# Performance work log

Hardware: AMD Instinct MI355X
Metric: run time of the kernel (lower is better)

The kernel has to match this reference:

```python
import jax, jax.numpy as jnp
import numpy as np

H, W = 5, 11          # fixed spatial map from ConvLSTM2D((5,11), ...)
P = H * W             # 55 pixels; 1x1 convs are per-pixel linear layers
HC = 64               # hidden channels
IC = 2                # input channels
FC_DIMS = [2 * HC * P, 3400, 1000, 500, 50]  # 7040 -> 3400 -> 1000 -> 500 -> 50


def setup_inputs() -> dict:
    key = jax.random.key(0)
    ks = jax.random.split(key, 24)
    B, T = 32, 256
    s = 0.05
    d = {}
    d["x1"] = jax.random.normal(ks[0], (B, T, IC, H, W), jnp.float32)
    d["x2"] = jax.random.normal(ks[1], (B, T, IC, H, W), jnp.float32)
    # ConvLSTM cell params: 1x1 convs fused into (in, 4*HC) matrices, gate order i,f,o,g
    d["wx1"] = jax.random.normal(ks[2], (IC, 4 * HC), jnp.float32) * s
    d["wh1"] = jax.random.normal(ks[3], (HC, 4 * HC), jnp.float32) * s
    d["bx1"] = jax.random.normal(ks[4], (4 * HC,), jnp.float32) * s
    d["bh1"] = jax.random.normal(ks[5], (4 * HC,), jnp.float32) * s
    d["wx2"] = jax.random.normal(ks[6], (IC, 4 * HC), jnp.float32) * s
    d["wh2"] = jax.random.normal(ks[7], (HC, 4 * HC), jnp.float32) * s
    d["bx2"] = jax.random.normal(ks[8], (4 * HC,), jnp.float32) * s
    d["bh2"] = jax.random.normal(ks[9], (4 * HC,), jnp.float32) * s
    # FC stack (stored as (in,out) so y = x @ W + b, equivalent to torch Linear)
    for i in range(4):
        fan_in, fan_out = FC_DIMS[i], FC_DIMS[i + 1]
        lim = 1.0 / np.sqrt(fan_in)
        d[f"fw{i+2}"] = jax.random.uniform(ks[10 + 2 * i], (fan_in, fan_out), jnp.float32, -lim, lim)
        d[f"fb{i+2}"] = jax.random.uniform(ks[11 + 2 * i], (fan_out,), jnp.float32, -lim, lim)
    return d


def _cell_step(h, c, gx, wh, bh):
    # gx: (B,P,4*HC) precomputed x contribution; h,c: (B,P,HC)
    g = gx + h @ wh + bh
    i, f, o, gg = jnp.split(g, 4, axis=-1)
    c = jax.nn.sigmoid(f) * c + jax.nn.sigmoid(i) * jnp.tanh(gg)
    h = jax.nn.sigmoid(o) * jnp.tanh(c)
    return h, c


def _sub_forward(x, wx1, wh1, bx1, bh1, wx2, wh2, bx2, bh2,
                 fw2, fb2, fw3, fb3, fw4, fb4, fw5, fb5):
    B, T = x.shape[0], x.shape[1]
    # (B,T,C,H,W) -> (B,T,P,C): pixels become a batch dim for the 1x1 convs
    xs = x.transpose(0, 1, 3, 4, 2).reshape(B, T, P, IC)
    # Precompute all input-to-gate projections once (big batched GEMM)
    gx1 = jnp.einsum('btpc,cd->btpd', xs, wx1) + bx1            # cell1: forward in time
    gx2 = jnp.einsum('btpc,cd->btpd', xs[:, ::-1], wx2) + bx2   # cell2: reversed in time
    h0 = jnp.zeros((B, P, HC), x.dtype)

    def step(carry, g):
        h1, c1, h2, c2 = carry
        g1, g2 = g
        h1, c1 = _cell_step(h1, c1, g1, wh1, bh1)
        h2, c2 = _cell_step(h2, c2, g2, wh2, bh2)
        return (h1, c1, h2, c2), None

    (h1, _, h2, _), _ = jax.lax.scan(
        step, (h0, h0, h0, h0),
        (gx1.transpose(1, 0, 2, 3), gx2.transpose(1, 0, 2, 3)))

    # torch.cat((h1,h2),1) on (B,HC,H,W) then flatten -> channel-major layout
    out = jnp.concatenate([h1.transpose(0, 2, 1), h2.transpose(0, 2, 1)], axis=1).reshape(B, -1)
    out = out @ fw2 + fb2
    out = out @ fw3 + fb3
    out = out @ fw4 + fb4
    out = out @ fw5 + fb5
    return out


def reference(x1, x2, wx1, wh1, bx1, bh1, wx2, wh2, bx2, bh2,
              fw2, fb2, fw3, fb3, fw4, fb4, fw5, fb5):
    args = (wx1, wh1, bx1, bh1, wx2, wh2, bx2, bh2,
            fw2, fb2, fw3, fb3, fw4, fb4, fw5, fb5)
    out1 = _sub_forward(x1, *args)
    out2 = _sub_forward(x2, *args)
    return (out1, out2)
```

## Files before the change

kernel.cpp:

```cpp
#include <hip/hip_runtime.h>


#define T_STEPS 256
#define PIX 55
#define MT 16
#define TILES 110
#define LOG2E 1.4426950408889634f
#define FC_SUB 128
#define FC_GRP 16

typedef float f32x4 __attribute__((ext_vector_type(4)));
typedef __bf16 bf16x8 __attribute__((ext_vector_type(8)));
typedef __bf16 bf16x4 __attribute__((ext_vector_type(4)));

__global__ __launch_bounds__(256) void lstm_kernel(
    const float* __restrict__ x1, const float* __restrict__ x2,
    const float* __restrict__ wx1, const float* __restrict__ wh1,
    const float* __restrict__ bx1, const float* __restrict__ bh1,
    const float* __restrict__ wx2, const float* __restrict__ wh2,
    const float* __restrict__ bx2, const float* __restrict__ bh2,
    float* __restrict__ feat)
{
    int bid  = blockIdx.x;
    int tile = bid % TILES;
    int cc   = bid / TILES;
    int sub  = cc >> 1, cell = cc & 1;
    const float* x  = sub  ? x2  : x1;
    const float* wx = cell ? wx2 : wx1;
    const float* wh = cell ? wh2 : wh1;
    const float* bx = cell ? bx2 : bx1;
    const float* bh = cell ? bh2 : bh1;

    int tid  = threadIdx.x;
    int w    = tid >> 6;
    int l    = tid & 63;
    int quad = l >> 4;
    int c16  = l & 15;

    __shared__ float xl[MT * 514];
    __shared__ __align__(16) __bf16 hb[2][2][MT][72];

    {
        int seq0 = tile * MT;
        for (int i = 0; i < 32; ++i) {
            int idx = tid + 256 * i;
            int m = idx >> 9;
            int tc = idx & 511;
            int t = tc >> 1, c = tc & 1;
            int seq = seq0 + m;
            int b = seq / PIX, p = seq % PIX;
            xl[m * 514 + tc] = x[((b * T_STEPS + t) * 2 + c) * PIX + p];
        }
    }
    {
        __bf16* hz = &hb[0][0][0][0];
        for (int i = tid; i < 2 * 2 * MT * 72; i += 256) hz[i] = (__bf16)0.0f;
    }

    bf16x8 Whi[4][2], Wlo[4][2];
    float btot[4][4], wxa[4][4], wxb[4][4];
#pragma unroll
    for (int g = 0; g < 4; ++g) {
        int col = 64 * g + 16 * w + c16;
#pragma unroll
        for (int r = 0; r < 4; ++r) {
            int u = 64 * g + 16 * w + 4 * quad + r;
            btot[g][r] = bx[u] + bh[u];
            wxa[g][r]  = wx[u];
            wxb[g][r]  = wx[256 + u];
        }
#pragma unroll
        for (int q = 0; q < 2; ++q) {
#pragma unroll
            for (int j = 0; j < 8; ++j) {
                int k = 32 * q + 8 * quad + j;
                float wv = wh[k * 256 + col];
                __bf16 hi = (__bf16)wv;
                Whi[g][q][j] = hi;
                Wlo[g][q][j] = (__bf16)(wv - (float)hi);
            }
        }
    }

    float cst[4]  = {0.f, 0.f, 0.f, 0.f};
    float hfin[4] = {0.f, 0.f, 0.f, 0.f};

    __syncthreads();
    float2 xv = *(const float2*)&xl[c16 * 514 + (cell ? (T_STEPS - 1) : 0) * 2];

#pragma unroll 2
    for (int t = 0; t < T_STEPS; ++t) {
        int rb = t & 1, wb = rb ^ 1;

        bf16x8 Bh[2], Bl[2];
#pragma unroll
        for (int q = 0; q < 2; ++q) {
            Bh[q] = *(const bf16x8*)&hb[rb][0][c16][32 * q + 8 * quad];
            Bl[q] = *(const bf16x8*)&hb[rb][1][c16][32 * q + 8 * quad];
        }

        f32x4 acc[4];
#pragma unroll
        for (int g = 0; g < 4; ++g) {
#pragma unroll
            for (int r = 0; r < 4; ++r)
                acc[g][r] = fmaf(xv.y, wxb[g][r], fmaf(xv.x, wxa[g][r], btot[g][r]));
        }
#pragma unroll
        for (int g = 0; g < 4; ++g)
            acc[g] = __builtin_amdgcn_mfma_f32_16x16x32_bf16(Whi[g][0], Bh[0], acc[g], 0, 0, 0);
#pragma unroll
        for (int g = 0; g < 4; ++g)
            acc[g] = __builtin_amdgcn_mfma_f32_16x16x32_bf16(Whi[g][1], Bh[1], acc[g], 0, 0, 0);
#pragma unroll
        for (int g = 0; g < 4; ++g)
            acc[g] = __builtin_amdgcn_mfma_f32_16x16x32_bf16(Wlo[g][0], Bh[0], acc[g], 0, 0, 0);
#pragma unroll
        for (int g = 0; g < 4; ++g)
            acc[g] = __builtin_amdgcn_mfma_f32_16x16x32_bf16(Wlo[g][1], Bh[1], acc[g], 0, 0, 0);
#pragma unroll
        for (int g = 0; g < 4; ++g)
            acc[g] = __builtin_amdgcn_mfma_f32_16x16x32_bf16(Whi[g][0], Bl[0], acc[g], 0, 0, 0);
#pragma unroll
        for (int g = 0; g < 4; ++g)
            acc[g] = __builtin_amdgcn_mfma_f32_16x16x32_bf16(Whi[g][1], Bl[1], acc[g], 0, 0, 0);

        float ei[4], ef[4], eo[4], eg[4];
#pragma unroll
        for (int r = 0; r < 4; ++r) {
            ei[r] = __builtin_amdgcn_exp2f(-LOG2E * acc[0][r]);
            ef[r] = __builtin_amdgcn_exp2f(-LOG2E * acc[1][r]);
            eo[r] = __builtin_amdgcn_exp2f(-LOG2E * acc[2][r]);
            eg[r] = __builtin_amdgcn_exp2f(-2.0f * LOG2E * acc[3][r]);
        }

        bf16x4 ph, pl;
#pragma unroll
        for (int r = 0; r < 4; ++r) {
            float sf  = __builtin_amdgcn_rcpf(1.0f + ef[r]);
            float itg = (1.0f - eg[r]) * __builtin_amdgcn_rcpf((1.0f + ei[r]) * (1.0f + eg[r]));
            float c   = fmaf(sf, cst[r], itg);
            cst[r] = c;
            float ec = __builtin_amdgcn_exp2f(-2.0f * LOG2E * c);
            float h  = (1.0f - ec) * __builtin_amdgcn_rcpf((1.0f + eo[r]) * (1.0f + ec));
            hfin[r] = h;
            __bf16 hi = (__bf16)h;
            ph[r] = hi;
            pl[r] = (__bf16)(h - (float)hi);
        }
        *(bf16x4*)&hb[wb][0][c16][16 * w + 4 * quad] = ph;
        *(bf16x4*)&hb[wb][1][c16][16 * w + 4 * quad] = pl;

        {
            int txn = (cell ? (T_STEPS - 2 - t) : (t + 1)) & 255;
            xv = *(const float2*)&xl[c16 * 514 + txn * 2];
        }
        __syncthreads();
    }

    {
        int seq = tile * MT + c16;
        int b = seq / PIX, p = seq % PIX;
#pragma unroll
        for (int r = 0; r < 4; ++r) {
            int u = 16 * w + 4 * quad + r;
            feat[(size_t)(sub * 32 + b) * 7040 + (cell * 64 + u) * PIX + p] = hfin[r];
        }
    }
}

__global__ __launch_bounds__(256) void fc_init(
    const float* __restrict__ b2, const float* __restrict__ b3,
    const float* __restrict__ b4, const float* __restrict__ b5,
    float* __restrict__ t1, float* __restrict__ t2,
    float* __restrict__ t3, float* __restrict__ o)
{
    int i = blockIdx.x * 256 + threadIdx.x;
    const int n1 = 64 * 3400, n2 = 64 * 1000, n3 = 64 * 500, n4 = 64 * 50;
    if (i < n1) { t1[i] = b2[i % 3400]; return; }
    i -= n1;
    if (i < n2) { t2[i] = b3[i % 1000]; return; }
    i -= n2;
    if (i < n3) { t3[i] = b4[i % 500]; return; }
    i -= n3;
    if (i < n4) { o[i] = b5[i % 50]; }
}

__global__ __launch_bounds__(256) void fc_gemm(const float* __restrict__ A,
                                               const float* __restrict__ W,
                                               float* __restrict__ out,
                                               int K, int N, int kchunk) {
    __shared__ __align__(16) float al[FC_SUB * 68];
    int tid = threadIdx.x;
    int l   = tid & 63;
    int wv  = tid >> 6;
    int k0   = blockIdx.y * kchunk;
    int kend = min(K, k0 + kchunk);

    int n  = blockIdx.x * 64 + l;
    int ne = min(n, N - 1);

    float acc[16];
#pragma unroll
    for (int i = 0; i < 16; ++i) acc[i] = 0.0f;

    for (int ks = k0; ks < kend; ks += FC_SUB) {
        int kcur = min(FC_SUB, kend - ks);
        __syncthreads();
        if (kcur == FC_SUB) {
#pragma unroll
            for (int i = 0; i < 32; ++i) {
                int idx = tid + 256 * i;
                int m = idx >> 7, kc = idx & 127;
                al[kc * 68 + m] = A[(size_t)m * K + ks + kc];
            }
        } else {
#pragma unroll
            for (int i = 0; i < 32; ++i) {
                int idx = tid + 256 * i;
                int m = idx >> 7, kc = idx & 127;
                if (kc < kcur) al[kc * 68 + m] = A[(size_t)m * K + ks + kc];
            }
        }
        __syncthreads();

        const float* wr = W + (size_t)ks * N + ne;
        if (kcur == FC_SUB) {
#pragma unroll
            for (int g8 = 0; g8 < FC_SUB / FC_GRP; ++g8) {
                float wbuf[FC_GRP];
#pragma unroll
                for (int j = 0; j < FC_GRP; ++j)
                    wbuf[j] = wr[(size_t)(g8 * FC_GRP + j) * N];
#pragma unroll
                for (int j = 0; j < FC_GRP; ++j) {
                    const float4* ap = (const float4*)&al[(g8 * FC_GRP + j) * 68 + 16 * wv];
#pragma unroll
                    for (int i = 0; i < 4; ++i) {
                        float4 a = ap[i];
                        acc[4 * i + 0] = fmaf(a.x, wbuf[j], acc[4 * i + 0]);
                        acc[4 * i + 1] = fmaf(a.y, wbuf[j], acc[4 * i + 1]);
                        acc[4 * i + 2] = fmaf(a.z, wbuf[j], acc[4 * i + 2]);
                        acc[4 * i + 3] = fmaf(a.w, wbuf[j], acc[4 * i + 3]);
                    }
                }
            }
        } else {
            int kc0 = 0;
            for (; kc0 + FC_GRP <= kcur; kc0 += FC_GRP) {
                float wbuf[FC_GRP];
#pragma unroll
                for (int j = 0; j < FC_GRP; ++j)
                    wbuf[j] = wr[(size_t)(kc0 + j) * N];
#pragma unroll
                for (int j = 0; j < FC_GRP; ++j) {
                    const float4* ap = (const float4*)&al[(kc0 + j) * 68 + 16 * wv];
#pragma unroll
                    for (int i = 0; i < 4; ++i) {
                        float4 a = ap[i];
                        acc[4 * i + 0] = fmaf(a.x, wbuf[j], acc[4 * i + 0]);
                        acc[4 * i + 1] = fmaf(a.y, wbuf[j], acc[4 * i + 1]);
                        acc[4 * i + 2] = fmaf(a.z, wbuf[j], acc[4 * i + 2]);
                        acc[4 * i + 3] = fmaf(a.w, wbuf[j], acc[4 * i + 3]);
                    }
                }
            }
            for (; kc0 < kcur; ++kc0) {
                float wvv = wr[(size_t)kc0 * N];
                const float4* ap = (const float4*)&al[kc0 * 68 + 16 * wv];
#pragma unroll
                for (int i = 0; i < 4; ++i) {
                    float4 a = ap[i];
                    acc[4 * i + 0] = fmaf(a.x, wvv, acc[4 * i + 0]);
                    acc[4 * i + 1] = fmaf(a.y, wvv, acc[4 * i + 1]);
                    acc[4 * i + 2] = fmaf(a.z, wvv, acc[4 * i + 2]);
                    acc[4 * i + 3] = fmaf(a.w, wvv, acc[4 * i + 3]);
                }
            }
        }
    }

    if (n < N) {
        float* pr = out + n;
#pragma unroll
        for (int i = 0; i < 16; ++i)
            unsafeAtomicAdd(&pr[(size_t)(16 * wv + i) * N], acc[i]);
    }
}

extern "C" void kernel_launch(void* const* d_in, const int* in_sizes, int n_in,
                              void* d_out, int out_size, void* d_ws, size_t ws_size,
                              hipStream_t stream) {
    const float* x1  = (const float*)d_in[0];
    const float* x2  = (const float*)d_in[1];
    const float* wx1 = (const float*)d_in[2];
    const float* wh1 = (const float*)d_in[3];
    const float* bx1 = (const float*)d_in[4];
    const float* bh1 = (const float*)d_in[5];
    const float* wx2 = (const float*)d_in[6];
    const float* wh2 = (const float*)d_in[7];
    const float* bx2 = (const float*)d_in[8];
    const float* bh2 = (const float*)d_in[9];
    const float* fw2 = (const float*)d_in[10];
    const float* fb2 = (const float*)d_in[11];
    const float* fw3 = (const float*)d_in[12];
    const float* fb3 = (const float*)d_in[13];
    const float* fw4 = (const float*)d_in[14];
    const float* fb4 = (const float*)d_in[15];
    const float* fw5 = (const float*)d_in[16];
    const float* fb5 = (const float*)d_in[17];

    char* ws = (char*)d_ws;
    float* feat = (float*)ws;
    float* t1   = feat + (size_t)64 * 7040;
    float* t2   = t1   + (size_t)64 * 3400;
    float* t3   = t2   + (size_t)64 * 1000;
    float* o    = (float*)d_out;

    fc_init<<<dim3(1238), dim3(256), 0, stream>>>(fb2, fb3, fb4, fb5, t1, t2, t3, o);

    lstm_kernel<<<dim3(440), dim3(256), 0, stream>>>(
        x1, x2, wx1, wh1, bx1, bh1, wx2, wh2, bx2, bh2, feat);

    fc_gemm<<<dim3(54, 28), dim3(256), 0, stream>>>(feat, fw2, t1, 7040, 3400, 256);
    fc_gemm<<<dim3(16, 54), dim3(256), 0, stream>>>(t1, fw3, t2, 3400, 1000, 64);
    fc_gemm<<<dim3(8, 16), dim3(256), 0, stream>>>(t2, fw4, t3, 1000, 500, 64);
    fc_gemm<<<dim3(1, 16), dim3(256), 0, stream>>>(t3, fw5, o, 500, 50, 32);
}
```

Baseline: 550.8 us.

## Halve LSTM block to two waves, each computing two 16-unit subtiles per gate

The recurrent LSTM kernel now runs with 128 threads (2 wavefronts) instead of 256. Each wave owns 32 hidden units per gate as two 16-column subtiles, which doubles the per-wave MFMA and activation work and the register-resident weights. The aim is to cut block-wide barrier cost per timestep and let the scheduler interleave independent MFMA chains. In exchange, register pressure doubles and per-step latency per wave grows, with fewer waves available to hide latency.

```diff
diff --git a/kernel.cpp b/kernel.cpp
--- a/kernel.cpp
+++ b/kernel.cpp
@@ -13,7 +13,7 @@
 typedef __bf16 bf16x8 __attribute__((ext_vector_type(8)));
 typedef __bf16 bf16x4 __attribute__((ext_vector_type(4)));
 
-__global__ __launch_bounds__(256) void lstm_kernel(
+__global__ __launch_bounds__(128, 1) void lstm_kernel(
     const float* __restrict__ x1, const float* __restrict__ x2,
     const float* __restrict__ wx1, const float* __restrict__ wh1,
     const float* __restrict__ bx1, const float* __restrict__ bh1,
@@ -32,7 +32,7 @@
     const float* bh = cell ? bh2 : bh1;
 
     int tid  = threadIdx.x;
-    int w    = tid >> 6;
+    int wv   = tid >> 6;
     int l    = tid & 63;
     int quad = l >> 4;
     int c16  = l & 15;
@@ -42,8 +42,8 @@
 
     {
         int seq0 = tile * MT;
-        for (int i = 0; i < 32; ++i) {
-            int idx = tid + 256 * i;
+        for (int i = 0; i < 64; ++i) {
+            int idx = tid + 128 * i;
             int m = idx >> 9;
             int tc = idx & 511;
             int t = tc >> 1, c = tc & 1;
@@ -54,36 +54,39 @@
     }
     {
         __bf16* hz = &hb[0][0][0][0];
-        for (int i = tid; i < 2 * 2 * MT * 72; i += 256) hz[i] = (__bf16)0.0f;
-    }
-
-    bf16x8 Whi[4][2], Wlo[4][2];
-    float btot[4][4], wxa[4][4], wxb[4][4];
+        for (int i = tid; i < 2 * 2 * MT * 72; i += 128) hz[i] = (__bf16)0.0f;
+    }
+
+    bf16x8 Whi[4][2][2], Wlo[4][2][2];
+    float btot[4][2][4], wxa[4][2][4], wxb[4][2][4];
 #pragma unroll
     for (int g = 0; g < 4; ++g) {
-        int col = 64 * g + 16 * w + c16;
-#pragma unroll
-        for (int r = 0; r < 4; ++r) {
-            int u = 64 * g + 16 * w + 4 * quad + r;
-            btot[g][r] = bx[u] + bh[u];
-            wxa[g][r]  = wx[u];
-            wxb[g][r]  = wx[256 + u];
-        }
-#pragma unroll
-        for (int q = 0; q < 2; ++q) {
-#pragma unroll
-            for (int j = 0; j < 8; ++j) {
-                int k = 32 * q + 8 * quad + j;
-                float wv = wh[k * 256 + col];
-                __bf16 hi = (__bf16)wv;
-                Whi[g][q][j] = hi;
-                Wlo[g][q][j] = (__bf16)(wv - (float)hi);
-            }
-        }
-    }
-
-    float cst[4]  = {0.f, 0.f, 0.f, 0.f};
-    float hfin[4] = {0.f, 0.f, 0.f, 0.f};
+#pragma unroll
+        for (int s = 0; s < 2; ++s) {
+            int col = 64 * g + 32 * wv + 16 * s + c16;
+#pragma unroll
+            for (int r = 0; r < 4; ++r) {
+                int u = 64 * g + 32 * wv + 16 * s + 4 * quad + r;
+                btot[g][s][r] = bx[u] + bh[u];
+                wxa[g][s][r]  = wx[u];
+                wxb[g][s][r]  = wx[256 + u];
+            }
+#pragma unroll
+            for (int q = 0; q < 2; ++q) {
+#pragma unroll
+                for (int j = 0; j < 8; ++j) {
+                    int k = 32 * q + 8 * quad + j;
+                    float wvv = wh[k * 256 + col];
+                    __bf16 hi = (__bf16)wvv;
+                    Whi[g][s][q][j] = hi;
+                    Wlo[g][s][q][j] = (__bf16)(wvv - (float)hi);
+                }
+            }
+        }
+    }
+
+    float cst[2][4]  = {{0.f, 0.f, 0.f, 0.f}, {0.f, 0.f, 0.f, 0.f}};
+    float hfin[2][4] = {{0.f, 0.f, 0.f, 0.f}, {0.f, 0.f, 0.f, 0.f}};
 
     __syncthreads();
     float2 xv = *(const float2*)&xl[c16 * 514 + (cell ? (T_STEPS - 1) : 0) * 2];
@@ -99,57 +102,80 @@
             Bl[q] = *(const bf16x8*)&hb[rb][1][c16][32 * q + 8 * quad];
         }
 
-        f32x4 acc[4];
-#pragma unroll
-        for (int g = 0; g < 4; ++g) {
-#pragma unroll
-            for (int r = 0; r < 4; ++r)
-                acc[g][r] = fmaf(xv.y, wxb[g][r], fmaf(xv.x, wxa[g][r], btot[g][r]));
-        }
-#pragma unroll
-        for (int g = 0; g < 4; ++g)
-            acc[g] = __builtin_amdgcn_mfma_f32_16x16x32_bf16(Whi[g][0], Bh[0], acc[g], 0, 0, 0);
-#pragma unroll
-        for (int g = 0; g < 4; ++g)
-            acc[g] = __builtin_amdgcn_mfma_f32_16x16x32_bf16(Whi[g][1], Bh[1], acc[g], 0, 0, 0);
-#pragma unroll
-        for (int g = 0; g < 4; ++g)
-            acc[g] = __builtin_amdgcn_mfma_f32_16x16x32_bf16(Wlo[g][0], Bh[0], acc[g], 0, 0, 0);
-#pragma unroll
-        for (int g = 0; g < 4; ++g)
-            acc[g] = __builtin_amdgcn_mfma_f32_16x16x32_bf16(Wlo[g][1], Bh[1], acc[g], 0, 0, 0);
-#pragma unroll
-        for (int g = 0; g < 4; ++g)
-            acc[g] = __builtin_amdgcn_mfma_f32_16x16x32_bf16(Whi[g][0], Bl[0], acc[g], 0, 0, 0);
-#pragma unroll
-        for (int g = 0; g < 4; ++g)
-            acc[g] = __builtin_amdgcn_mfma_f32_16x16x32_bf16(Whi[g][1], Bl[1], acc[g], 0, 0, 0);
-
-        float ei[4], ef[4], eo[4], eg[4];
-#pragma unroll
-        for (int r = 0; r < 4; ++r) {
-            ei[r] = __builtin_amdgcn_exp2f(-LOG2E * acc[0][r]);
-            ef[r] = __builtin_amdgcn_exp2f(-LOG2E * acc[1][r]);
-            eo[r] = __builtin_amdgcn_exp2f(-LOG2E * acc[2][r]);
-            eg[r] = __builtin_amdgcn_exp2f(-2.0f * LOG2E * acc[3][r]);
-        }
-
-        bf16x4 ph, pl;
-#pragma unroll
-        for (int r = 0; r < 4; ++r) {
-            float sf  = __builtin_amdgcn_rcpf(1.0f + ef[r]);
-            float itg = (1.0f - eg[r]) * __builtin_amdgcn_rcpf((1.0f + ei[r]) * (1.0f + eg[r]));
-            float c   = fmaf(sf, cst[r], itg);
-            cst[r] = c;
-            float ec = __builtin_amdgcn_exp2f(-2.0f * LOG2E * c);
-            float h  = (1.0f - ec) * __builtin_amdgcn_rcpf((1.0f + eo[r]) * (1.0f + ec));
-            hfin[r] = h;
-            __bf16 hi = (__bf16)h;
-            ph[r] = hi;
-            pl[r] = (__bf16)(h - (float)hi);
-        }
-        *(bf16x4*)&hb[wb][0][c16][16 * w + 4 * quad] = ph;
-        *(bf16x4*)&hb[wb][1][c16][16 * w + 4 * quad] = pl;
+        f32x4 acc[4][2];
+#pragma unroll
+        for (int g = 0; g < 4; ++g)
+#pragma unroll
+            for (int s = 0; s < 2; ++s)
+#pragma unroll
+                for (int r = 0; r < 4; ++r)
+                    acc[g][s][r] = fmaf(xv.y, wxb[g][s][r],
+                                        fmaf(xv.x, wxa[g][s][r], btot[g][s][r]));
+
+#pragma unroll
+        for (int g = 0; g < 4; ++g)
+#pragma unroll
+            for (int s = 0; s < 2; ++s)
+                acc[g][s] = __builtin_amdgcn_mfma_f32_16x16x32_bf16(Whi[g][s][0], Bh[0], acc[g][s], 0, 0, 0);
+#pragma unroll
+        for (int g = 0; g < 4; ++g)
+#pragma unroll
+            for (int s = 0; s < 2; ++s)
+                acc[g][s] = __builtin_amdgcn_mfma_f32_16x16x32_bf16(Whi[g][s][1], Bh[1], acc[g][s], 0, 0, 0);
+#pragma unroll
+        for (int g = 0; g < 4; ++g)
+#pragma unroll
+            for (int s = 0; s < 2; ++s)
+                acc[g][s] = __builtin_amdgcn_mfma_f32_16x16x32_bf16(Wlo[g][s][0], Bh[0], acc[g][s], 0, 0, 0);
+#pragma unroll
+        for (int g = 0; g < 4; ++g)
+#pragma unroll
+            for (int s = 0; s < 2; ++s)
+                acc[g][s] = __builtin_amdgcn_mfma_f32_16x16x32_bf16(Wlo[g][s][1], Bh[1], acc[g][s], 0, 0, 0);
+#pragma unroll
+        for (int g = 0; g < 4; ++g)
+#pragma unroll
+            for (int s = 0; s < 2; ++s)
+                acc[g][s] = __builtin_amdgcn_mfma_f32_16x16x32_bf16(Whi[g][s][0], Bl[0], acc[g][s], 0, 0, 0);
+#pragma unroll
+        for (int g = 0; g < 4; ++g)
+#pragma unroll
+            for (int s = 0; s < 2; ++s)
+                acc[g][s] = __builtin_amdgcn_mfma_f32_16x16x32_bf16(Whi[g][s][1], Bl[1], acc[g][s], 0, 0, 0);
+
+        float ei[2][4], ef[2][4], eo[2][4], eg[2][4];
+#pragma unroll
+        for (int s = 0; s < 2; ++s)
+#pragma unroll
+            for (int r = 0; r < 4; ++r) {
+                ei[s][r] = __builtin_amdgcn_exp2f(-LOG2E * acc[0][s][r]);
+                ef[s][r] = __builtin_amdgcn_exp2f(-LOG2E * acc[1][s][r]);
+                eo[s][r] = __builtin_amdgcn_exp2f(-LOG2E * acc[2][s][r]);
+                eg[s][r] = __builtin_amdgcn_exp2f(-2.0f * LOG2E * acc[3][s][r]);
+            }
+
+        bf16x4 ph[2], pl[2];
+#pragma unroll
+        for (int s = 0; s < 2; ++s)
+#pragma unroll
+            for (int r = 0; r < 4; ++r) {
+                float sf  = __builtin_amdgcn_rcpf(1.0f + ef[s][r]);
+                float itg = (1.0f - eg[s][r]) *
+                            __builtin_amdgcn_rcpf((1.0f + ei[s][r]) * (1.0f + eg[s][r]));
+                float c   = fmaf(sf, cst[s][r], itg);
+                cst[s][r] = c;
+                float ec = __builtin_amdgcn_exp2f(-2.0f * LOG2E * c);
+                float h  = (1.0f - ec) * __builtin_amdgcn_rcpf((1.0f + eo[s][r]) * (1.0f + ec));
+                hfin[s][r] = h;
+                __bf16 hi = (__bf16)h;
+                ph[s][r] = hi;
+                pl[s][r] = (__bf16)(h - (float)hi);
+            }
+#pragma unroll
+        for (int s = 0; s < 2; ++s) {
+            *(bf16x4*)&hb[wb][0][c16][32 * wv + 16 * s + 4 * quad] = ph[s];
+            *(bf16x4*)&hb[wb][1][c16][32 * wv + 16 * s + 4 * quad] = pl[s];
+        }
 
         {
             int txn = (cell ? (T_STEPS - 2 - t) : (t + 1)) & 255;
@@ -162,10 +188,12 @@
         int seq = tile * MT + c16;
         int b = seq / PIX, p = seq % PIX;
 #pragma unroll
-        for (int r = 0; r < 4; ++r) {
-            int u = 16 * w + 4 * quad + r;
-            feat[(size_t)(sub * 32 + b) * 7040 + (cell * 64 + u) * PIX + p] = hfin[r];
-        }
+        for (int s = 0; s < 2; ++s)
+#pragma unroll
+            for (int r = 0; r < 4; ++r) {
+                int u = 32 * wv + 16 * s + 4 * quad + r;
+                feat[(size_t)(sub * 32 + b) * 7040 + (cell * 64 + u) * PIX + p] = hfin[s][r];
+            }
     }
 }
 
@@ -319,7 +347,7 @@
 
     fc_init<<<dim3(1238), dim3(256), 0, stream>>>(fb2, fb3, fb4, fb5, t1, t2, t3, o);
 
-    lstm_kernel<<<dim3(440), dim3(256), 0, stream>>>(
+    lstm_kernel<<<dim3(440), dim3(128), 0, stream>>>(
         x1, x2, wx1, wh1, bx1, bh1, wx2, wh2, bx2, bh2, feat);
 
     fc_gemm<<<dim3(54, 28), dim3(256), 0, stream>>>(feat, fw2, t1, 7040, 3400, 256);
```

Measured after the change: 585.0 us. 6.2% more time.

## Fold bias-init into LSTM launch and prescale gate weights by exp constants

Applied to the files above, without the earlier changes.

Drops the separate fc_init kernel by adding 10 extra blocks to the LSTM launch that write the FC bias broadcasts with a grid-stride loop, saving one launch. Also folds the -log2e and -2*log2e sigmoid/tanh scaling into the recurrent weights, input weights and biases at load time, which removes four multiplies per gate element from the serial recurrence. Prescaling changes how the split bf16 hi/lo weights round, with a small numerical difference. The init blocks take CU slots alongside the 440 LSTM blocks.

```diff
diff --git a/kernel.cpp b/kernel.cpp
--- a/kernel.cpp
+++ b/kernel.cpp
@@ -5,6 +5,8 @@
 #define PIX 55
 #define MT 16
 #define TILES 110
+#define LSTM_BLOCKS 440
+#define INIT_BLOCKS 10
 #define LOG2E 1.4426950408889634f
 #define FC_SUB 128
 #define FC_GRP 16
@@ -19,9 +21,31 @@
     const float* __restrict__ bx1, const float* __restrict__ bh1,
     const float* __restrict__ wx2, const float* __restrict__ wh2,
     const float* __restrict__ bx2, const float* __restrict__ bh2,
-    float* __restrict__ feat)
+    float* __restrict__ feat,
+    const float* __restrict__ fb2, const float* __restrict__ fb3,
+    const float* __restrict__ fb4, const float* __restrict__ fb5,
+    float* __restrict__ t1, float* __restrict__ t2,
+    float* __restrict__ t3, float* __restrict__ o)
 {
     int bid  = blockIdx.x;
+    int tid  = threadIdx.x;
+
+    if (bid >= LSTM_BLOCKS) {
+        int base = (bid - LSTM_BLOCKS) * 256 + tid;
+        const int n1 = 64 * 3400, n2 = 64 * 1000, n3 = 64 * 500, n4 = 64 * 50;
+        const int tot = n1 + n2 + n3 + n4;
+        for (int i = base; i < tot; i += 256 * INIT_BLOCKS) {
+            int j = i;
+            if (j < n1) { t1[j] = fb2[j % 3400]; continue; }
+            j -= n1;
+            if (j < n2) { t2[j] = fb3[j % 1000]; continue; }
+            j -= n2;
+            if (j < n3) { t3[j] = fb4[j % 500]; continue; }
+            o[j - n3] = fb5[(j - n3) % 50];
+        }
+        return;
+    }
+
     int tile = bid % TILES;
     int cc   = bid / TILES;
     int sub  = cc >> 1, cell = cc & 1;
@@ -31,7 +55,6 @@
     const float* bx = cell ? bx2 : bx1;
     const float* bh = cell ? bh2 : bh1;
 
-    int tid  = threadIdx.x;
     int w    = tid >> 6;
     int l    = tid & 63;
     int quad = l >> 4;
@@ -61,20 +84,21 @@
     float btot[4][4], wxa[4][4], wxb[4][4];
 #pragma unroll
     for (int g = 0; g < 4; ++g) {
+        float sg = (g == 3) ? (-2.0f * LOG2E) : (-LOG2E);
         int col = 64 * g + 16 * w + c16;
 #pragma unroll
         for (int r = 0; r < 4; ++r) {
             int u = 64 * g + 16 * w + 4 * quad + r;
-            btot[g][r] = bx[u] + bh[u];
-            wxa[g][r]  = wx[u];
-            wxb[g][r]  = wx[256 + u];
+            btot[g][r] = sg * (bx[u] + bh[u]);
+            wxa[g][r]  = sg * wx[u];
+            wxb[g][r]  = sg * wx[256 + u];
         }
 #pragma unroll
         for (int q = 0; q < 2; ++q) {
 #pragma unroll
             for (int j = 0; j < 8; ++j) {
                 int k = 32 * q + 8 * quad + j;
-                float wv = wh[k * 256 + col];
+                float wv = sg * wh[k * 256 + col];
                 __bf16 hi = (__bf16)wv;
                 Whi[g][q][j] = hi;
                 Wlo[g][q][j] = (__bf16)(wv - (float)hi);
@@ -128,10 +152,10 @@
         float ei[4], ef[4], eo[4], eg[4];
 #pragma unroll
         for (int r = 0; r < 4; ++r) {
-            ei[r] = __builtin_amdgcn_exp2f(-LOG2E * acc[0][r]);
-            ef[r] = __builtin_amdgcn_exp2f(-LOG2E * acc[1][r]);
-            eo[r] = __builtin_amdgcn_exp2f(-LOG2E * acc[2][r]);
-            eg[r] = __builtin_amdgcn_exp2f(-2.0f * LOG2E * acc[3][r]);
+            ei[r] = __builtin_amdgcn_exp2f(acc[0][r]);
+            ef[r] = __builtin_amdgcn_exp2f(acc[1][r]);
+            eo[r] = __builtin_amdgcn_exp2f(acc[2][r]);
+            eg[r] = __builtin_amdgcn_exp2f(acc[3][r]);
         }
 
         bf16x4 ph, pl;
@@ -167,23 +191,6 @@
             feat[(size_t)(sub * 32 + b) * 7040 + (cell * 64 + u) * PIX + p] = hfin[r];
         }
     }
-}
-
-__global__ __launch_bounds__(256) void fc_init(
-    const float* __restrict__ b2, const float* __restrict__ b3,
-    const float* __restrict__ b4, const float* __restrict__ b5,
-    float* __restrict__ t1, float* __restrict__ t2,
-    float* __restrict__ t3, float* __restrict__ o)
-{
-    int i = blockIdx.x * 256 + threadIdx.x;
-    const int n1 = 64 * 3400, n2 = 64 * 1000, n3 = 64 * 500, n4 = 64 * 50;
-    if (i < n1) { t1[i] = b2[i % 3400]; return; }
-    i -= n1;
-    if (i < n2) { t2[i] = b3[i % 1000]; return; }
-    i -= n2;
-    if (i < n3) { t3[i] = b4[i % 500]; return; }
-    i -= n3;
-    if (i < n4) { o[i] = b5[i % 50]; }
 }
 
 __global__ __launch_bounds__(256) void fc_gemm(const float* __restrict__ A,
@@ -317,10 +324,9 @@
     float* t3   = t2   + (size_t)64 * 1000;
     float* o    = (float*)d_out;
 
-    fc_init<<<dim3(1238), dim3(256), 0, stream>>>(fb2, fb3, fb4, fb5, t1, t2, t3, o);
-
-    lstm_kernel<<<dim3(440), dim3(256), 0, stream>>>(
-        x1, x2, wx1, wh1, bx1, bh1, wx2, wh2, bx2, bh2, feat);
+    lstm_kernel<<<dim3(LSTM_BLOCKS + INIT_BLOCKS), dim3(256), 0, stream>>>(
+        x1, x2, wx1, wh1, bx1, bh1, wx2, wh2, bx2, bh2, feat,
+        fb2, fb3, fb4, fb5, t1, t2, t3, o);
 
     fc_gemm<<<dim3(54, 28), dim3(256), 0, stream>>>(feat, fw2, t1, 7040, 3400, 256);
     fc_gemm<<<dim3(16, 54), dim3(256), 0, stream>>>(t1, fw3, t2, 3400, 1000, 64);
```

After: 535.9 us. 1.03x faster.
